# Performance work log

Measured on AMD Instinct MI355X. Metric: run time of the kernel, lower is better.

The kernel has to match this reference:

```python
import jax, jax.numpy as jnp
import numpy as np

N, T, C = 8, 2048, 1024   # batch, seq_len, n_embd (== num_cls)
NUM_CLS = 1024
LID, TL = 6, 12


def setup_inputs() -> dict:
    key = jax.random.key(0)
    ks = jax.random.split(key, 5)
    s = 1.0 / np.sqrt(C)
    x = jax.random.normal(ks[0], (N, T, C), jnp.float32)
    Wk = jax.random.normal(ks[1], (C, C), jnp.float32) * s
    Wv = jax.random.normal(ks[2], (C, C), jnp.float32) * s
    Wr = jax.random.normal(ks[3], (C, C), jnp.float32) * s
    Wo = jax.random.normal(ks[4], (NUM_CLS, C), jnp.float32) * s
    # faithful time-parameter initialization from __init__
    r0 = LID / (TL - 1)            # ratio_0_to_1
    r1 = 1.0 - LID / TL            # ratio_1_to_almost0
    ddd = (np.arange(C, dtype=np.float32) / C).reshape(1, 1, C)
    time_mix_k = jnp.asarray(ddd ** r1)
    time_mix_v = jnp.asarray(ddd ** r1 + 0.3 * r0)
    time_mix_r = jnp.asarray(ddd ** (0.5 * r1))
    time_decay = jnp.zeros((C,), jnp.float32)                 # decay_speed init
    time_first = jnp.full((C,), np.log(0.3), jnp.float32)
    last_x = jnp.zeros((N, 1, C), jnp.float32)                # init_x repeated
    state = jnp.zeros((N, 3, 1, C), jnp.float32)              # init_state repeated
    return {"x": x, "it": 0, "Wk": Wk, "Wv": Wv, "Wr": Wr, "Wo": Wo,
            "time_mix_k": time_mix_k, "time_mix_v": time_mix_v,
            "time_mix_r": time_mix_r, "time_decay": time_decay,
            "time_first": time_first, "last_x": last_x, "state": state}


def _wkv_with_eps(w, u, k, v, state):
    """Numerically-stabilized RWKV wkv scan. k,v: (N,T,C); state: (N,3,1,C)."""
    alpha = state[:, 0, -1]  # (N,C)
    beta = state[:, 1, -1]
    eps = state[:, 2, -1]

    def step(carry, kv):
        a, b, e = carry
        kt, vt = kv                      # each (N,C)
        ukt = u + kt
        tau = jnp.maximum(ukt, e)
        e1 = jnp.exp(e - tau)
        e2 = jnp.exp(ukt - tau)
        wkv_t = (e1 * a + e2 * vt) / (e1 * b + e2)
        w_eps = e - w
        e_n = jnp.maximum(w_eps, kt)
        e1n = jnp.exp(w_eps - e_n)
        e2n = jnp.exp(kt - e_n)
        return (e1n * a + e2n * vt, e1n * b + e2n, e_n), wkv_t

    kT = jnp.swapaxes(k, 0, 1)  # (T,N,C)
    vT = jnp.swapaxes(v, 0, 1)
    (alpha, beta, eps), wkv = jax.lax.scan(step, (alpha, beta, eps), (kT, vT))
    wkv = jnp.swapaxes(wkv, 0, 1)  # (N,T,C)
    last_state = jnp.stack([alpha, beta, eps], axis=1)[:, :, None, :]  # (N,3,1,C)
    return wkv, last_state


def reference(x, it, Wk, Wv, Wr, Wo, time_mix_k, time_mix_v, time_mix_r,
              time_decay, time_first, last_x, state):
    # time-mix blend (last_x = init_x zeros, broadcast over T as in the source)
    k = (x * time_mix_k + last_x * (1.0 - time_mix_k)) @ Wk.T
    v = (x * time_mix_v + last_x * (1.0 - time_mix_v)) @ Wv.T
    r = (x * time_mix_r + last_x * (1.0 - time_mix_r)) @ Wr.T
    sr = jax.nn.sigmoid(r)
    w = jnp.exp(time_decay)
    u = time_first
    wkv, _last_state = _wkv_with_eps(w, u, k, v, state)
    rwkv = (wkv * sr) @ Wo.T  # (N,T,NUM_CLS)
    return rwkv
```

## Files before the change

kernel.cpp:

```cpp
#include <hip/hip_runtime.h>
#include <hip/hip_bf16.h>
#include <stdint.h>


typedef float f4 __attribute__((ext_vector_type(4)));
typedef short bh8 __attribute__((ext_vector_type(8)));
typedef unsigned int u32;
typedef unsigned short u16;

__device__ __forceinline__ u32 cvt2bf(float a, float b) {
    __hip_bfloat162 h = __float22bfloat162_rn(make_float2(a, b));
    u32 u; __builtin_memcpy(&u, &h, 4); return u;
}
__device__ __forceinline__ float b2f(u16 u) {
    u32 x = (u32)u << 16; float f; __builtin_memcpy(&f, &x, 4); return f;
}
__device__ __forceinline__ u16 f2b(float f) {
    __hip_bfloat16 h = __float2bfloat16(f);
    u16 u; __builtin_memcpy(&u, &h, 2); return u;
}
__device__ __forceinline__ void gld_lds16(const void* g, void* l) {
    __builtin_amdgcn_global_load_lds(
        (const __attribute__((address_space(1))) u32*)g,
        (__attribute__((address_space(3))) u32*)l, 16, 0, 0);
}

__device__ __forceinline__ void gemm_core(
    const u16* __restrict__ A, const u16* __restrict__ B,
    int m0, int n0, u16* As, u16* Bs, f4 (&acc)[4][4])
{
    const int tid  = threadIdx.x;
    const int w    = tid >> 6;
    const int lane = tid & 63;

    const int srow = w * 32 + (lane >> 2);
    const int slot = lane & 3;
    const int chk  = slot ^ ((srow >> 1) & 3);
    const u16* gA0 = A + (size_t)(m0 + srow) * 1024 + chk * 8;
    const u16* gA1 = gA0 + (size_t)16 * 1024;
    const u16* gB0 = B + (size_t)(n0 + srow) * 1024 + chk * 8;
    const u16* gB1 = gB0 + (size_t)16 * 1024;
    u16* lA0 = As + (w * 32) * 32;
    u16* lA1 = lA0 + 16 * 32;
    u16* lB0 = Bs + (w * 32) * 32;
    u16* lB1 = lB0 + 16 * 32;

    const int fr   = lane & 15;
    const int quad = lane >> 4;
    const int wm = (w & 1) * 64;
    const int wn = (w >> 1) * 64;
    const int sp = quad ^ ((fr >> 1) & 3);
    const int aoff = (wm + fr) * 32 + sp * 8;
    const int boff = (wn + fr) * 32 + sp * 8;

    for (int kk = 0; kk < 1024; kk += 32) {
        gld_lds16(gA0 + kk, lA0);
        gld_lds16(gA1 + kk, lA1);
        gld_lds16(gB0 + kk, lB0);
        gld_lds16(gB1 + kk, lB1);
        __syncthreads();
        bh8 af[4], bf[4];
#pragma unroll
        for (int i = 0; i < 4; i++) af[i] = *(const bh8*)(As + aoff + i * 16 * 32);
#pragma unroll
        for (int j = 0; j < 4; j++) bf[j] = *(const bh8*)(Bs + boff + j * 16 * 32);
#pragma unroll
        for (int i = 0; i < 4; i++)
#pragma unroll
            for (int j = 0; j < 4; j++)
                acc[i][j] = __builtin_amdgcn_mfma_f32_16x16x32_bf16(af[i], bf[j], acc[i][j], 0, 0, 0);
        __syncthreads();
    }
}

__global__ __launch_bounds__(256, 2) void gemm_kvr(
    const u16* __restrict__ A, const u16* __restrict__ Wall, const float* __restrict__ bias,
    u16* __restrict__ Kb, u16* __restrict__ Vb, u16* __restrict__ SRb)
{
    __shared__ __align__(16) u16 As[128 * 32];
    __shared__ __align__(16) u16 Bs[128 * 32];
    const int m0 = blockIdx.x * 128;
    const int proj = blockIdx.y >> 3;
    const int n0 = (blockIdx.y & 7) * 128;
    const u16* B = Wall + (size_t)proj * 1048576;

    f4 acc[4][4];
#pragma unroll
    for (int i = 0; i < 4; i++)
#pragma unroll
        for (int j = 0; j < 4; j++) { f4 z = {0.f, 0.f, 0.f, 0.f}; acc[i][j] = z; }
    gemm_core(A, B, m0, n0, As, Bs, acc);

    u16* Y = proj == 0 ? Kb : (proj == 1 ? Vb : SRb);
    const int lane = threadIdx.x & 63;
    const int w = threadIdx.x >> 6;
    const int fr = lane & 15, quad = lane >> 4;
    const int wm = (w & 1) * 64, wn = (w >> 1) * 64;
    const int rb = quad * 4;
    const int batch = m0 >> 11;
    float bv[4];
#pragma unroll
    for (int j = 0; j < 4; j++) bv[j] = bias[proj * 8192 + batch * 1024 + n0 + wn + j * 16 + fr];
#pragma unroll
    for (int i = 0; i < 4; i++)
#pragma unroll
        for (int j = 0; j < 4; j++)
#pragma unroll
            for (int r = 0; r < 4; r++) {
                float v = acc[i][j][r] + bv[j];
                if (proj == 2) v = __fdividef(1.0f, 1.0f + __expf(-v));
                size_t row = (size_t)(m0 + wm + i * 16 + rb + r);
                size_t col = (size_t)(n0 + wn + j * 16 + fr);
                Y[row * 1024 + col] = f2b(v);
            }
}

__global__ __launch_bounds__(256, 2) void gemm_out(
    const u16* __restrict__ A, const u16* __restrict__ B, float* __restrict__ Y)
{
    __shared__ __align__(16) u16 As[128 * 32];
    __shared__ __align__(16) u16 Bs[128 * 32];
    const int m0 = blockIdx.x * 128;
    const int n0 = blockIdx.y * 128;
    f4 acc[4][4];
#pragma unroll
    for (int i = 0; i < 4; i++)
#pragma unroll
        for (int j = 0; j < 4; j++) { f4 z = {0.f, 0.f, 0.f, 0.f}; acc[i][j] = z; }
    gemm_core(A, B, m0, n0, As, Bs, acc);

    const int lane = threadIdx.x & 63;
    const int w = threadIdx.x >> 6;
    const int fr = lane & 15, quad = lane >> 4;
    const int wm = (w & 1) * 64, wn = (w >> 1) * 64;
    const int rb = quad * 4;
#pragma unroll
    for (int i = 0; i < 4; i++)
#pragma unroll
        for (int j = 0; j < 4; j++)
#pragma unroll
            for (int r = 0; r < 4; r++) {
                size_t row = (size_t)(m0 + wm + i * 16 + rb + r);
                size_t col = (size_t)(n0 + wn + j * 16 + fr);
                Y[row * 1024 + col] = acc[i][j][r];
            }
}

__global__ __launch_bounds__(256) void convx(const float* __restrict__ s, u16* __restrict__ d) {
    int idx = blockIdx.x * 256 + threadIdx.x;
    int e = idx << 2;
    f4 v = *(const f4*)(s + e);
    *(uint2*)(d + e) = make_uint2(cvt2bf(v.x, v.y), cvt2bf(v.z, v.w));
}

__global__ __launch_bounds__(256) void prepw(
    const float* __restrict__ Wk, const float* __restrict__ Wv,
    const float* __restrict__ Wr, const float* __restrict__ Wo,
    const float* __restrict__ tmk, const float* __restrict__ tmv, const float* __restrict__ tmr,
    u16* __restrict__ Wall)
{
    int idx = blockIdx.x * 256 + threadIdx.x;
    int e = idx << 2;
    int wid = e >> 20;
    int off = e & 1048575;
    int c = e & 1023;
    const float* src = wid == 0 ? Wk : (wid == 1 ? Wv : (wid == 2 ? Wr : Wo));
    f4 v = *(const f4*)(src + off);
    if (wid < 3) {
        const float* m = wid == 0 ? tmk : (wid == 1 ? tmv : tmr);
        v = v * *(const f4*)(m + c);
    }
    *(uint2*)(Wall + e) = make_uint2(cvt2bf(v.x, v.y), cvt2bf(v.z, v.w));
}

__global__ __launch_bounds__(256) void bias3(
    const float* __restrict__ Wk, const float* __restrict__ Wv, const float* __restrict__ Wr,
    const float* __restrict__ tmk, const float* __restrict__ tmv, const float* __restrict__ tmr,
    const float* __restrict__ lastx, float* __restrict__ bias)
{
    int wid = blockIdx.x * 4 + (threadIdx.x >> 6);
    int lane = threadIdx.x & 63;
    int proj = wid >> 10;
    int n = wid & 1023;
    const float* W = proj == 0 ? Wk : (proj == 1 ? Wv : Wr);
    const float* m = proj == 0 ? tmk : (proj == 1 ? tmv : tmr);
    float acc[8];
#pragma unroll
    for (int b = 0; b < 8; b++) acc[b] = 0.f;
    for (int c = lane; c < 1024; c += 64) {
        float wc = W[n * 1024 + c] * (1.0f - m[c]);
#pragma unroll
        for (int b = 0; b < 8; b++) acc[b] = fmaf(lastx[b * 1024 + c], wc, acc[b]);
    }
#pragma unroll
    for (int b = 0; b < 8; b++) {
        float v = acc[b];
#pragma unroll
        for (int sh = 32; sh >= 1; sh >>= 1) v += __shfl_xor(v, sh);
        if (lane == 0) bias[proj * 8192 + b * 1024 + n] = v;
    }
}

__global__ __launch_bounds__(256) void wkv_pass1(
    const u16* __restrict__ Kp, const u16* __restrict__ Vp,
    const float* __restrict__ tdec,
    float* __restrict__ Ca, float* __restrict__ Cb, float* __restrict__ Ce)
{
    int tid = blockIdx.x * 256 + threadIdx.x;
    int c = (tid & 511) << 1;
    int chunk = (tid >> 9) & 31;
    int n = tid >> 14;
    float w0 = __expf(tdec[c]), w1 = __expf(tdec[c + 1]);
    int base = (n * 2048 + chunk * 64) * 1024 + c;
    float a0 = 0.f, b0 = 0.f, e0 = -1e30f;
    float a1 = 0.f, b1 = 0.f, e1 = -1e30f;
#pragma unroll 4
    for (int i = 0; i < 64; i++) {
        u32 ku = *(const u32*)(Kp + base + (i << 10));
        u32 vu = *(const u32*)(Vp + base + (i << 10));
        float k0 = b2f((u16)ku), k1 = b2f((u16)(ku >> 16));
        float v0 = b2f((u16)vu), v1 = b2f((u16)(vu >> 16));
        float en0 = fmaxf(e0 - w0, k0);
        float f10 = __expf(e0 - w0 - en0), f20 = __expf(k0 - en0);
        a0 = fmaf(f10, a0, f20 * v0); b0 = fmaf(f10, b0, f20); e0 = en0;
        float en1 = fmaxf(e1 - w1, k1);
        float f11 = __expf(e1 - w1 - en1), f21 = __expf(k1 - en1);
        a1 = fmaf(f11, a1, f21 * v1); b1 = fmaf(f11, b1, f21); e1 = en1;
    }
    int oidx = ((n * 32 + chunk) << 10) + c;
    *(float2*)(Ca + oidx) = make_float2(a0, a1);
    *(float2*)(Cb + oidx) = make_float2(b0, b1);
    *(float2*)(Ce + oidx) = make_float2(e0, e1);
}

__global__ __launch_bounds__(256) void wkv_pass2(
    const float* __restrict__ state, const float* __restrict__ tdec,
    const float* __restrict__ Ca, const float* __restrict__ Cb, const float* __restrict__ Ce,
    float* __restrict__ Sa, float* __restrict__ Sb, float* __restrict__ Se)
{
    int tid = blockIdx.x * 256 + threadIdx.x;
    int c = tid & 1023;
    int n = tid >> 10;
    float a = state[(n * 3 + 0) * 1024 + c];
    float b = state[(n * 3 + 1) * 1024 + c];
    float e = state[(n * 3 + 2) * 1024 + c];
    float wL = __expf(tdec[c]) * 64.0f;
    for (int ch = 0; ch < 32; ++ch) {
        int idx = ((n * 32 + ch) << 10) + c;
        Sa[idx] = a; Sb[idx] = b; Se[idx] = e;
        float ce = Ce[idx];
        float en = fmaxf(e - wL, ce);
        float f1 = __expf(e - wL - en);
        float f2 = __expf(ce - en);
        a = fmaf(f1, a, f2 * Ca[idx]);
        b = fmaf(f1, b, f2 * Cb[idx]);
        e = en;
    }
}

__global__ __launch_bounds__(256) void wkv_pass3(
    const u16* __restrict__ Kp, const u16* __restrict__ Vp, const u16* __restrict__ SRp,
    const float* __restrict__ Sa, const float* __restrict__ Sb, const float* __restrict__ Se,
    const float* __restrict__ tfirst, const float* __restrict__ tdec,
    u16* __restrict__ Pp)
{
    int tid = blockIdx.x * 256 + threadIdx.x;
    int c = (tid & 511) << 1;
    int chunk = (tid >> 9) & 31;
    int n = tid >> 14;
    int sidx = ((n * 32 + chunk) << 10) + c;
    float a0 = Sa[sidx], b0 = Sb[sidx], e0 = Se[sidx];
    float a1 = Sa[sidx + 1], b1 = Sb[sidx + 1], e1 = Se[sidx + 1];
    float u0 = tfirst[c], u1 = tfirst[c + 1];
    float w0 = __expf(tdec[c]), w1 = __expf(tdec[c + 1]);
    int base = (n * 2048 + chunk * 64) * 1024 + c;
#pragma unroll 2
    for (int i = 0; i < 64; i++) {
        u32 ku = *(const u32*)(Kp + base + (i << 10));
        u32 vu = *(const u32*)(Vp + base + (i << 10));
        u32 su = *(const u32*)(SRp + base + (i << 10));
        float k0 = b2f((u16)ku), k1 = b2f((u16)(ku >> 16));
        float v0 = b2f((u16)vu), v1 = b2f((u16)(vu >> 16));
        float s0 = b2f((u16)su), s1 = b2f((u16)(su >> 16));
        float t0 = fmaxf(u0 + k0, e0);
        float x10 = __expf(e0 - t0), x20 = __expf(u0 + k0 - t0);
        float wkv0 = __fdividef(fmaf(x10, a0, x20 * v0), fmaf(x10, b0, x20));
        float t1 = fmaxf(u1 + k1, e1);
        float x11 = __expf(e1 - t1), x21 = __expf(u1 + k1 - t1);
        float wkv1 = __fdividef(fmaf(x11, a1, x21 * v1), fmaf(x11, b1, x21));
        *(u32*)(Pp + base + (i << 10)) = (u32)f2b(wkv0 * s0) | ((u32)f2b(wkv1 * s1) << 16);
        float en0 = fmaxf(e0 - w0, k0);
        float f10 = __expf(e0 - w0 - en0), f20 = __expf(k0 - en0);
        a0 = fmaf(f10, a0, f20 * v0); b0 = fmaf(f10, b0, f20); e0 = en0;
        float en1 = fmaxf(e1 - w1, k1);
        float f11 = __expf(e1 - w1 - en1), f21 = __expf(k1 - en1);
        a1 = fmaf(f11, a1, f21 * v1); b1 = fmaf(f11, b1, f21); e1 = en1;
    }
}

extern "C" void kernel_launch(void* const* d_in, const int* in_sizes, int n_in,
                              void* d_out, int out_size, void* d_ws, size_t ws_size,
                              hipStream_t stream) {
    const float* x      = (const float*)d_in[0];
    const float* Wk     = (const float*)d_in[2];
    const float* Wv     = (const float*)d_in[3];
    const float* Wr     = (const float*)d_in[4];
    const float* Wo     = (const float*)d_in[5];
    const float* tmk    = (const float*)d_in[6];
    const float* tmv    = (const float*)d_in[7];
    const float* tmr    = (const float*)d_in[8];
    const float* tdec   = (const float*)d_in[9];
    const float* tfirst = (const float*)d_in[10];
    const float* lastx  = (const float*)d_in[11];
    const float* state  = (const float*)d_in[12];
    float* out = (float*)d_out;

    const size_t MB = 1024ull * 1024ull;
    char* ws = (char*)d_ws;
    u16* Kb   = (u16*)(ws);
    u16* Vb   = (u16*)(ws + 32 * MB);
    u16* SRb  = (u16*)(ws + 64 * MB);
    u16* xb   = (u16*)(ws + 96 * MB);
    u16* Wall = (u16*)(ws + 128 * MB);
    float* bias = (float*)(ws + 136 * MB);
    float* Ca = (float*)(ws + 137 * MB);
    float* Cb = Ca + 262144;
    float* Ce = Cb + 262144;
    float* Sa = Ce + 262144;
    float* Sb = Sa + 262144;
    float* Se = Sb + 262144;
    u16* Pb = xb;

    dim3 blk(256);
    convx<<<16384, blk, 0, stream>>>(x, xb);
    prepw<<<4096, blk, 0, stream>>>(Wk, Wv, Wr, Wo, tmk, tmv, tmr, Wall);
    bias3<<<768, blk, 0, stream>>>(Wk, Wv, Wr, tmk, tmv, tmr, lastx, bias);
    gemm_kvr<<<dim3(128, 24), blk, 0, stream>>>(xb, Wall, bias, Kb, Vb, SRb);
    wkv_pass1<<<512, blk, 0, stream>>>(Kb, Vb, tdec, Ca, Cb, Ce);
    wkv_pass2<<<32, blk, 0, stream>>>(state, tdec, Ca, Cb, Ce, Sa, Sb, Se);
    wkv_pass3<<<512, blk, 0, stream>>>(Kb, Vb, SRb, Sa, Sb, Se, tfirst, tdec, Pb);
    gemm_out<<<dim3(128, 8), blk, 0, stream>>>(Pb, Wall + 3145728, out);
}
```

Baseline: 377.3 us.

## Stage GEMM epilogues through LDS, fuse prep kernels, halve WKV chunk length

The K/V/SR and output GEMM epilogues now stage results in shared memory so global stores are wide and coalesced instead of scattered 2-byte or 4-byte writes. Occupancy hints rise to 4 blocks per SM, and the grid is reordered so blocks sharing an M tile run together. The three prep kernels are merged into one launch. The WKV chunked scan uses 64 chunks of 32 steps instead of 32 of 64 for more parallelism, and pass2 writes prefix states in place. The trade-offs are more LDS use per block and a longer serial pass2.

```diff
diff --git a/kernel.cpp b/kernel.cpp
--- a/kernel.cpp
+++ b/kernel.cpp
@@ -73,15 +73,17 @@
     }
 }
 
-__global__ __launch_bounds__(256, 2) void gemm_kvr(
+__global__ __launch_bounds__(256, 4) void gemm_kvr(
     const u16* __restrict__ A, const u16* __restrict__ Wall, const float* __restrict__ bias,
     u16* __restrict__ Kb, u16* __restrict__ Vb, u16* __restrict__ SRb)
 {
-    __shared__ __align__(16) u16 As[128 * 32];
-    __shared__ __align__(16) u16 Bs[128 * 32];
-    const int m0 = blockIdx.x * 128;
-    const int proj = blockIdx.y >> 3;
-    const int n0 = (blockIdx.y & 7) * 128;
+    __shared__ __align__(16) char pool[33792];
+    u16* As = (u16*)pool;
+    u16* Bs = (u16*)(pool + 8192);
+
+    const int proj = blockIdx.x >> 3;
+    const int n0 = (blockIdx.x & 7) * 128;
+    const int m0 = blockIdx.y * 128;
     const u16* B = Wall + (size_t)proj * 1048576;
 
     f4 acc[4][4];
@@ -101,6 +103,8 @@
     float bv[4];
 #pragma unroll
     for (int j = 0; j < 4; j++) bv[j] = bias[proj * 8192 + batch * 1024 + n0 + wn + j * 16 + fr];
+
+    u16* S = (u16*)pool;
 #pragma unroll
     for (int i = 0; i < 4; i++)
 #pragma unroll
@@ -109,19 +113,31 @@
             for (int r = 0; r < 4; r++) {
                 float v = acc[i][j][r] + bv[j];
                 if (proj == 2) v = __fdividef(1.0f, 1.0f + __expf(-v));
-                size_t row = (size_t)(m0 + wm + i * 16 + rb + r);
-                size_t col = (size_t)(n0 + wn + j * 16 + fr);
-                Y[row * 1024 + col] = f2b(v);
+                int row = wm + i * 16 + rb + r;
+                int col = wn + j * 16 + fr;
+                S[row * 132 + col] = f2b(v);
             }
-}
-
-__global__ __launch_bounds__(256, 2) void gemm_out(
+    __syncthreads();
+    const int ch = lane & 15;
+#pragma unroll
+    for (int t = 0; t < 8; t++) {
+        int lrow = w * 32 + t * 4 + (lane >> 4);
+        const u16* p = S + lrow * 132 + ch * 8;
+        uint2 lo = *(const uint2*)p;
+        uint2 hi = *(const uint2*)(p + 4);
+        uint4 val = make_uint4(lo.x, lo.y, hi.x, hi.y);
+        *(uint4*)(Y + (size_t)(m0 + lrow) * 1024 + n0 + ch * 8) = val;
+    }
+}
+
+__global__ __launch_bounds__(256, 4) void gemm_out(
     const u16* __restrict__ A, const u16* __restrict__ B, float* __restrict__ Y)
 {
-    __shared__ __align__(16) u16 As[128 * 32];
-    __shared__ __align__(16) u16 Bs[128 * 32];
-    const int m0 = blockIdx.x * 128;
-    const int n0 = blockIdx.y * 128;
+    __shared__ __align__(16) char pool[33792];
+    u16* As = (u16*)pool;
+    u16* Bs = (u16*)(pool + 8192);
+    const int n0 = blockIdx.x * 128;
+    const int m0 = blockIdx.y * 128;
     f4 acc[4][4];
 #pragma unroll
     for (int i = 0; i < 4; i++)
@@ -132,72 +148,77 @@
     const int lane = threadIdx.x & 63;
     const int w = threadIdx.x >> 6;
     const int fr = lane & 15, quad = lane >> 4;
-    const int wm = (w & 1) * 64, wn = (w >> 1) * 64;
+    const int wn = (w >> 1) * 64;
     const int rb = quad * 4;
-#pragma unroll
-    for (int i = 0; i < 4; i++)
+    float* Sf = (float*)pool;
+#pragma unroll
+    for (int i = 0; i < 4; i++) {
+        __syncthreads();
 #pragma unroll
         for (int j = 0; j < 4; j++)
 #pragma unroll
             for (int r = 0; r < 4; r++) {
-                size_t row = (size_t)(m0 + wm + i * 16 + rb + r);
-                size_t col = (size_t)(n0 + wn + j * 16 + fr);
-                Y[row * 1024 + col] = acc[i][j][r];
+                int lrow = (w & 1) * 16 + rb + r;
+                Sf[lrow * 132 + wn + j * 16 + fr] = acc[i][j][r];
             }
-}
-
-__global__ __launch_bounds__(256) void convx(const float* __restrict__ s, u16* __restrict__ d) {
-    int idx = blockIdx.x * 256 + threadIdx.x;
-    int e = idx << 2;
-    f4 v = *(const f4*)(s + e);
-    *(uint2*)(d + e) = make_uint2(cvt2bf(v.x, v.y), cvt2bf(v.z, v.w));
-}
-
-__global__ __launch_bounds__(256) void prepw(
+        __syncthreads();
+#pragma unroll
+        for (int t = 0; t < 4; t++) {
+            int lrow = w * 8 + t * 2 + (lane >> 5);
+            int ch = lane & 31;
+            f4 val = *(const f4*)(Sf + lrow * 132 + ch * 4);
+            int g = m0 + ((lrow >> 4) << 6) + i * 16 + (lrow & 15);
+            *(f4*)(Y + (size_t)g * 1024 + n0 + ch * 4) = val;
+        }
+    }
+}
+
+__global__ __launch_bounds__(256) void prep_all(
+    const float* __restrict__ x, const float* __restrict__ lastx,
     const float* __restrict__ Wk, const float* __restrict__ Wv,
     const float* __restrict__ Wr, const float* __restrict__ Wo,
     const float* __restrict__ tmk, const float* __restrict__ tmv, const float* __restrict__ tmr,
-    u16* __restrict__ Wall)
-{
-    int idx = blockIdx.x * 256 + threadIdx.x;
-    int e = idx << 2;
-    int wid = e >> 20;
-    int off = e & 1048575;
-    int c = e & 1023;
-    const float* src = wid == 0 ? Wk : (wid == 1 ? Wv : (wid == 2 ? Wr : Wo));
-    f4 v = *(const f4*)(src + off);
-    if (wid < 3) {
-        const float* m = wid == 0 ? tmk : (wid == 1 ? tmv : tmr);
-        v = v * *(const f4*)(m + c);
-    }
-    *(uint2*)(Wall + e) = make_uint2(cvt2bf(v.x, v.y), cvt2bf(v.z, v.w));
-}
-
-__global__ __launch_bounds__(256) void bias3(
-    const float* __restrict__ Wk, const float* __restrict__ Wv, const float* __restrict__ Wr,
-    const float* __restrict__ tmk, const float* __restrict__ tmv, const float* __restrict__ tmr,
-    const float* __restrict__ lastx, float* __restrict__ bias)
-{
-    int wid = blockIdx.x * 4 + (threadIdx.x >> 6);
-    int lane = threadIdx.x & 63;
-    int proj = wid >> 10;
-    int n = wid & 1023;
-    const float* W = proj == 0 ? Wk : (proj == 1 ? Wv : Wr);
-    const float* m = proj == 0 ? tmk : (proj == 1 ? tmv : tmr);
-    float acc[8];
-#pragma unroll
-    for (int b = 0; b < 8; b++) acc[b] = 0.f;
-    for (int c = lane; c < 1024; c += 64) {
-        float wc = W[n * 1024 + c] * (1.0f - m[c]);
-#pragma unroll
-        for (int b = 0; b < 8; b++) acc[b] = fmaf(lastx[b * 1024 + c], wc, acc[b]);
-    }
-#pragma unroll
-    for (int b = 0; b < 8; b++) {
-        float v = acc[b];
-#pragma unroll
-        for (int sh = 32; sh >= 1; sh >>= 1) v += __shfl_xor(v, sh);
-        if (lane == 0) bias[proj * 8192 + b * 1024 + n] = v;
+    u16* __restrict__ xb, u16* __restrict__ Wall, float* __restrict__ bias)
+{
+    int b = blockIdx.x;
+    if (b < 16384) {
+        int e = (b * 256 + threadIdx.x) << 2;
+        f4 v = *(const f4*)(x + e);
+        *(uint2*)(xb + e) = make_uint2(cvt2bf(v.x, v.y), cvt2bf(v.z, v.w));
+    } else if (b < 20480) {
+        int e = ((b - 16384) * 256 + threadIdx.x) << 2;
+        int wid = e >> 20;
+        int off = e & 1048575;
+        int c = e & 1023;
+        const float* src = wid == 0 ? Wk : (wid == 1 ? Wv : (wid == 2 ? Wr : Wo));
+        f4 v = *(const f4*)(src + off);
+        if (wid < 3) {
+            const float* m = wid == 0 ? tmk : (wid == 1 ? tmv : tmr);
+            v = v * *(const f4*)(m + c);
+        }
+        *(uint2*)(Wall + e) = make_uint2(cvt2bf(v.x, v.y), cvt2bf(v.z, v.w));
+    } else {
+        int wid = (b - 20480) * 4 + (threadIdx.x >> 6);
+        int lane = threadIdx.x & 63;
+        int proj = wid >> 10;
+        int n = wid & 1023;
+        const float* W = proj == 0 ? Wk : (proj == 1 ? Wv : Wr);
+        const float* m = proj == 0 ? tmk : (proj == 1 ? tmv : tmr);
+        float acc[8];
+#pragma unroll
+        for (int bb = 0; bb < 8; bb++) acc[bb] = 0.f;
+        for (int c = lane; c < 1024; c += 64) {
+            float wc = W[n * 1024 + c] * (1.0f - m[c]);
+#pragma unroll
+            for (int bb = 0; bb < 8; bb++) acc[bb] = fmaf(lastx[bb * 1024 + c], wc, acc[bb]);
+        }
+#pragma unroll
+        for (int bb = 0; bb < 8; bb++) {
+            float v = acc[bb];
+#pragma unroll
+            for (int sh = 32; sh >= 1; sh >>= 1) v += __shfl_xor(v, sh);
+            if (lane == 0) bias[proj * 8192 + bb * 1024 + n] = v;
+        }
     }
 }
 
@@ -208,14 +229,14 @@
 {
     int tid = blockIdx.x * 256 + threadIdx.x;
     int c = (tid & 511) << 1;
-    int chunk = (tid >> 9) & 31;
-    int n = tid >> 14;
+    int chunk = (tid >> 9) & 63;
+    int n = tid >> 15;
     float w0 = __expf(tdec[c]), w1 = __expf(tdec[c + 1]);
-    int base = (n * 2048 + chunk * 64) * 1024 + c;
+    int base = (n * 2048 + chunk * 32) * 1024 + c;
     float a0 = 0.f, b0 = 0.f, e0 = -1e30f;
     float a1 = 0.f, b1 = 0.f, e1 = -1e30f;
 #pragma unroll 4
-    for (int i = 0; i < 64; i++) {
+    for (int i = 0; i < 32; i++) {
         u32 ku = *(const u32*)(Kp + base + (i << 10));
         u32 vu = *(const u32*)(Vp + base + (i << 10));
         float k0 = b2f((u16)ku), k1 = b2f((u16)(ku >> 16));
@@ -227,7 +248,7 @@
         float f11 = __expf(e1 - w1 - en1), f21 = __expf(k1 - en1);
         a1 = fmaf(f11, a1, f21 * v1); b1 = fmaf(f11, b1, f21); e1 = en1;
     }
-    int oidx = ((n * 32 + chunk) << 10) + c;
+    int oidx = ((n * 64 + chunk) << 10) + c;
     *(float2*)(Ca + oidx) = make_float2(a0, a1);
     *(float2*)(Cb + oidx) = make_float2(b0, b1);
     *(float2*)(Ce + oidx) = make_float2(e0, e1);
@@ -235,8 +256,7 @@
 
 __global__ __launch_bounds__(256) void wkv_pass2(
     const float* __restrict__ state, const float* __restrict__ tdec,
-    const float* __restrict__ Ca, const float* __restrict__ Cb, const float* __restrict__ Ce,
-    float* __restrict__ Sa, float* __restrict__ Sb, float* __restrict__ Se)
+    float* Ca, float* Cb, float* Ce)
 {
     int tid = blockIdx.x * 256 + threadIdx.x;
     int c = tid & 1023;
@@ -244,16 +264,16 @@
     float a = state[(n * 3 + 0) * 1024 + c];
     float b = state[(n * 3 + 1) * 1024 + c];
     float e = state[(n * 3 + 2) * 1024 + c];
-    float wL = __expf(tdec[c]) * 64.0f;
-    for (int ch = 0; ch < 32; ++ch) {
-        int idx = ((n * 32 + ch) << 10) + c;
-        Sa[idx] = a; Sb[idx] = b; Se[idx] = e;
-        float ce = Ce[idx];
+    float wL = __expf(tdec[c]) * 32.0f;
+    for (int ch = 0; ch < 64; ++ch) {
+        int idx = ((n * 64 + ch) << 10) + c;
+        float ca = Ca[idx], cb = Cb[idx], ce = Ce[idx];
+        Ca[idx] = a; Cb[idx] = b; Ce[idx] = e;
         float en = fmaxf(e - wL, ce);
         float f1 = __expf(e - wL - en);
         float f2 = __expf(ce - en);
-        a = fmaf(f1, a, f2 * Ca[idx]);
-        b = fmaf(f1, b, f2 * Cb[idx]);
+        a = fmaf(f1, a, f2 * ca);
+        b = fmaf(f1, b, f2 * cb);
         e = en;
     }
 }
@@ -266,16 +286,16 @@
 {
     int tid = blockIdx.x * 256 + threadIdx.x;
     int c = (tid & 511) << 1;
-    int chunk = (tid >> 9) & 31;
-    int n = tid >> 14;
-    int sidx = ((n * 32 + chunk) << 10) + c;
+    int chunk = (tid >> 9) & 63;
+    int n = tid >> 15;
+    int sidx = ((n * 64 + chunk) << 10) + c;
     float a0 = Sa[sidx], b0 = Sb[sidx], e0 = Se[sidx];
     float a1 = Sa[sidx + 1], b1 = Sb[sidx + 1], e1 = Se[sidx + 1];
     float u0 = tfirst[c], u1 = tfirst[c + 1];
     float w0 = __expf(tdec[c]), w1 = __expf(tdec[c + 1]);
-    int base = (n * 2048 + chunk * 64) * 1024 + c;
+    int base = (n * 2048 + chunk * 32) * 1024 + c;
 #pragma unroll 2
-    for (int i = 0; i < 64; i++) {
+    for (int i = 0; i < 32; i++) {
         u32 ku = *(const u32*)(Kp + base + (i << 10));
         u32 vu = *(const u32*)(Vp + base + (i << 10));
         u32 su = *(const u32*)(SRp + base + (i << 10));
@@ -324,20 +344,15 @@
     u16* Wall = (u16*)(ws + 128 * MB);
     float* bias = (float*)(ws + 136 * MB);
     float* Ca = (float*)(ws + 137 * MB);
-    float* Cb = Ca + 262144;
-    float* Ce = Cb + 262144;
-    float* Sa = Ce + 262144;
-    float* Sb = Sa + 262144;
-    float* Se = Sb + 262144;
+    float* Cb = (float*)(ws + 139 * MB);
+    float* Ce = (float*)(ws + 141 * MB);
     u16* Pb = xb;
 
     dim3 blk(256);
-    convx<<<16384, blk, 0, stream>>>(x, xb);
-    prepw<<<4096, blk, 0, stream>>>(Wk, Wv, Wr, Wo, tmk, tmv, tmr, Wall);
-    bias3<<<768, blk, 0, stream>>>(Wk, Wv, Wr, tmk, tmv, tmr, lastx, bias);
-    gemm_kvr<<<dim3(128, 24), blk, 0, stream>>>(xb, Wall, bias, Kb, Vb, SRb);
-    wkv_pass1<<<512, blk, 0, stream>>>(Kb, Vb, tdec, Ca, Cb, Ce);
-    wkv_pass2<<<32, blk, 0, stream>>>(state, tdec, Ca, Cb, Ce, Sa, Sb, Se);
-    wkv_pass3<<<512, blk, 0, stream>>>(Kb, Vb, SRb, Sa, Sb, Se, tfirst, tdec, Pb);
-    gemm_out<<<dim3(128, 8), blk, 0, stream>>>(Pb, Wall + 3145728, out);
-}
+    prep_all<<<21248, blk, 0, stream>>>(x, lastx, Wk, Wv, Wr, Wo, tmk, tmv, tmr, xb, Wall, bias);
+    gemm_kvr<<<dim3(24, 128), blk, 0, stream>>>(xb, Wall, bias, Kb, Vb, SRb);
+    wkv_pass1<<<1024, blk, 0, stream>>>(Kb, Vb, tdec, Ca, Cb, Ce);
+    wkv_pass2<<<32, blk, 0, stream>>>(state, tdec, Ca, Cb, Ce);
+    wkv_pass3<<<1024, blk, 0, stream>>>(Kb, Vb, SRb, Ca, Cb, Ce, tfirst, tdec, Pb);
+    gemm_out<<<dim3(8, 128), blk, 0, stream>>>(Pb, Wall + 3145728, out);
+}
```

New measurement: 387.1 us. 1.03x slower.
